# Kernel tuning notes

Measured on AMD Instinct MI355X. Metric: run time of the kernel, lower is better.

The kernel has to match this reference:

```python
import jax, jax.numpy as jnp
import numpy as np

N_NODES = 50000
N_EDGES = 1600000
D_IN = 128
D_HID = 128
D_OUT = 3
EPS = 1e-5


def setup_inputs() -> dict:
    key = jax.random.key(0)
    ks = jax.random.split(key, 16)
    def lin(k, fi, fo):
        s = 1.0 / np.sqrt(fi)
        return jax.random.uniform(k, (fi, fo), jnp.float32, -s, s)
    inp = {
        "x": jax.random.normal(ks[0], (N_NODES, D_IN), jnp.float32),
        "edge_index": jax.random.randint(ks[1], (2, N_EDGES), 0, N_NODES, jnp.int32),
        "W1": lin(ks[2], D_IN, D_HID), "b1": jnp.zeros((D_HID,), jnp.float32),
        "W2": lin(ks[3], D_HID, D_HID), "b2": jnp.zeros((D_HID,), jnp.float32),
        "W3": lin(ks[4], D_HID, D_HID), "b3": jnp.zeros((D_HID,), jnp.float32),
        "g1": jnp.ones((D_HID,), jnp.float32), "beta1": jnp.zeros((D_HID,), jnp.float32),
        "g2": jnp.ones((D_HID,), jnp.float32), "beta2": jnp.zeros((D_HID,), jnp.float32),
        "Wp1": lin(ks[5], D_HID, D_HID), "bp1": jnp.zeros((D_HID,), jnp.float32),
        "Wp2": lin(ks[6], D_HID, D_OUT), "bp2": jnp.zeros((D_OUT,), jnp.float32),
    }
    return inp


def _gcn_norm(edge_index, n):
    # add self-loops, symmetric normalization (PyG GCNConv default)
    loops = jnp.arange(n, dtype=edge_index.dtype)
    row = jnp.concatenate([edge_index[0], loops])  # source
    col = jnp.concatenate([edge_index[1], loops])  # target
    deg = jax.ops.segment_sum(jnp.ones_like(col, jnp.float32), col, num_segments=n)
    dinv = jnp.where(deg > 0, jax.lax.rsqrt(deg), 0.0)
    norm = dinv[row] * dinv[col]  # [E+N]
    return row, col, norm


def _gcn_conv(x, W, b, row, col, norm, n):
    h = x @ W                                # [N, F]
    msg = h[row] * norm[:, None]             # [E+N, F] gather
    out = jax.ops.segment_sum(msg, col, num_segments=n)  # scatter-add
    return out + b


def _layernorm(x, g, beta):
    mu = jnp.mean(x, axis=-1, keepdims=True)
    var = jnp.var(x, axis=-1, keepdims=True)
    return (x - mu) * jax.lax.rsqrt(var + EPS) * g + beta


def reference(x, edge_index, W1, b1, W2, b2, W3, b3, g1, beta1, g2, beta2, Wp1, bp1, Wp2, bp2):
    n = x.shape[0]
    row, col, norm = _gcn_norm(edge_index, n)
    # layer 0
    h = _gcn_conv(x, W1, b1, row, col, norm, n)
    h = _layernorm(jax.nn.relu(h), g1, beta1)  # dropout = identity (eval mode)
    # layer 1
    h = _gcn_conv(h, W2, b2, row, col, norm, n)
    h = _layernorm(jax.nn.relu(h), g2, beta2)
    # layer 2 (no layernorm)
    h = _gcn_conv(h, W3, b3, row, col, norm, n)
    h = jax.nn.relu(h)
    # post-MP MLP head (dropout = identity in eval)
    h = h @ Wp1 + bp1
    return h @ Wp2 + bp2
```

## Files before the change

### kernel.cpp

```cpp
#include <hip/hip_runtime.h>
#include <hip/hip_bf16.h>

#define EPS_LN 1e-5f
#define NB    256
#define SEGCAP 16384

typedef int ivec4 __attribute__((ext_vector_type(4)));


__global__ __launch_bounds__(256) void bucket_hist(const int* __restrict__ col,
                                                   int* __restrict__ chunkBH,
                                                   int E, int per, int nbuck) {
    __shared__ int hist[256];
    int t = threadIdx.x;
    hist[t] = 0;
    __syncthreads();
    int s0 = blockIdx.x * per;
    int s1 = s0 + per; if (s1 > E) s1 = E;
    if (s0 < s1) {
        int q0 = s0 >> 2, q1 = s1 >> 2;
        for (int i = q0 + t; i < q1; i += 256) {
            ivec4 c = __builtin_nontemporal_load((const ivec4*)col + i);
            atomicAdd(&hist[c.x >> 8], 1);
            atomicAdd(&hist[c.y >> 8], 1);
            atomicAdd(&hist[c.z >> 8], 1);
            atomicAdd(&hist[c.w >> 8], 1);
        }
        for (int i = (q1 << 2) + t; i < s1; i += 256)
            atomicAdd(&hist[col[i] >> 8], 1);
    }
    __syncthreads();
    if (t < nbuck) chunkBH[blockIdx.x * 256 + t] = hist[t];
}

__global__ __launch_bounds__(256) void bucket_scan(int* __restrict__ chunkBH,
                                                   int* __restrict__ bucketStart,
                                                   int* __restrict__ rowPtr,
                                                   int E, int n, int nbuck, int nb) {
    __shared__ int tot[256];
    int t = threadIdx.x;
    int run = 0;
    if (t < nbuck) {
        for (int k0 = 0; k0 < nb; k0 += 16) {
            int v[16];
#pragma unroll
            for (int j = 0; j < 16; j++)
                v[j] = (k0 + j < nb) ? chunkBH[(k0 + j) * 256 + t] : 0;
#pragma unroll
            for (int j = 0; j < 16; j++) {
                int tv = v[j];
                if (k0 + j < nb) chunkBH[(k0 + j) * 256 + t] = run;
                run += tv;
            }
        }
    }
    tot[t] = run;
    __syncthreads();
    for (int d = 1; d < 256; d <<= 1) {
        int add = (t >= d) ? tot[t - d] : 0;
        __syncthreads();
        tot[t] += add;
        __syncthreads();
    }
    if (t < nbuck) bucketStart[t] = tot[t] - run;
    if (t == 0) { bucketStart[nbuck] = E; rowPtr[n] = E; }
}

__global__ __launch_bounds__(256) void scatter_pairs(const int* __restrict__ row,
                                                     const int* __restrict__ col,
                                                     const int* __restrict__ chunkBH,
                                                     const int* __restrict__ bucketStart,
                                                     unsigned long long* __restrict__ tmp,
                                                     int E, int per, int nbuck) {
    __shared__ int curs[256];
    int t = threadIdx.x;
    int k = blockIdx.x;
    curs[t] = (t < nbuck) ? (chunkBH[k * 256 + t] + bucketStart[t]) : 0;
    __syncthreads();
    int s0 = k * per;
    int s1 = s0 + per; if (s1 > E) s1 = E;
    if (s0 >= s1) return;
    int q0 = s0 >> 2, q1 = s1 >> 2;
    for (int i = q0 + t; i < q1; i += 256) {
        ivec4 c4 = __builtin_nontemporal_load((const ivec4*)col + i);
        ivec4 r4 = __builtin_nontemporal_load((const ivec4*)row + i);
        int p0 = atomicAdd(&curs[c4.x >> 8], 1);
        tmp[p0] = ((unsigned long long)(unsigned)c4.x << 32) | (unsigned)r4.x;
        int p1 = atomicAdd(&curs[c4.y >> 8], 1);
        tmp[p1] = ((unsigned long long)(unsigned)c4.y << 32) | (unsigned)r4.y;
        int p2 = atomicAdd(&curs[c4.z >> 8], 1);
        tmp[p2] = ((unsigned long long)(unsigned)c4.z << 32) | (unsigned)r4.z;
        int p3 = atomicAdd(&curs[c4.w >> 8], 1);
        tmp[p3] = ((unsigned long long)(unsigned)c4.w << 32) | (unsigned)r4.w;
    }
    for (int i = (q1 << 2) + t; i < s1; i += 256) {
        int c = col[i], r = row[i];
        int p = atomicAdd(&curs[c >> 8], 1);
        tmp[p] = ((unsigned long long)(unsigned)c << 32) | (unsigned)r;
    }
}

__global__ __launch_bounds__(256) void bucket_fill(const unsigned long long* __restrict__ tmp,
                                                   const int* __restrict__ bucketStart,
                                                   int* __restrict__ rowPtr,
                                                   float* __restrict__ dinv,
                                                   int* __restrict__ srcList,
                                                   int n) {
    __shared__ int cnt[256];
    __shared__ int cur[256];
    __shared__ int seg[SEGCAP];
    int b = blockIdx.x, t = threadIdx.x;
    int node0 = b << 8;
    int s0 = bucketStart[b], s1 = bucketStart[b + 1];
    int len = s1 - s0;
    cnt[t] = 0;
    __syncthreads();
    for (int i = s0 + t; i < s1; i += 256) {
        int c = (int)(tmp[i] >> 32);
        atomicAdd(&cnt[c - node0], 1);
    }
    __syncthreads();
    int v = cnt[t];
    cur[t] = v;
    __syncthreads();
    for (int d = 1; d < 256; d <<= 1) {
        int add = (t >= d) ? cur[t - d] : 0;
        __syncthreads();
        cur[t] += add;
        __syncthreads();
    }
    int excl = cur[t] - v;
    int node = node0 + t;
    if (node < n) {
        rowPtr[node] = s0 + excl;
        dinv[node] = rsqrtf((float)v + 1.0f);
    }
    cur[t] = excl;
    __syncthreads();
    if (len <= SEGCAP) {
        for (int i = s0 + t; i < s1; i += 256) {
            unsigned long long p = tmp[i];
            int c = (int)(p >> 32);
            int r = (int)(p & 0xffffffffu);
            int pos = atomicAdd(&cur[c - node0], 1);
            seg[pos] = r;
        }
        __syncthreads();
        for (int i = t; i < len; i += 256)
            srcList[s0 + i] = seg[i];
    } else {
        for (int i = s0 + t; i < s1; i += 256) {
            unsigned long long p = tmp[i];
            int c = (int)(p >> 32);
            int r = (int)(p & 0xffffffffu);
            int pos = atomicAdd(&cur[c - node0], 1);
            srcList[s0 + pos] = r;
        }
    }
}

__global__ __launch_bounds__(256) void gemm_hb(const float* __restrict__ A,
                                               const float* __restrict__ W,
                                               const float* __restrict__ dinv,
                                               unsigned short* __restrict__ Cb,
                                               int n) {
    __shared__ float As[16][68];
    __shared__ float Ws[16][144];

    const int tx = threadIdx.x;
    const int row0 = blockIdx.x * 64;
    const int jg = (tx & 15) * 8;
    const int ig = (tx >> 4) * 4;
    const int js = jg + ((jg >> 5) << 2);

    const int ar  = tx >> 2;
    const int ac4 = (tx & 3) * 4;
    const int growA = row0 + ar;
    const float* Ap = A + (size_t)growA * 128 + ac4;

    float acc[4][8];
#pragma unroll
    for (int r = 0; r < 4; r++)
#pragma unroll
        for (int c = 0; c < 8; c++) acc[r][c] = 0.f;

    for (int k0 = 0; k0 < 128; k0 += 16) {
        float4 va = make_float4(0.f, 0.f, 0.f, 0.f);
        if (growA < n) va = *(const float4*)(Ap + k0);
        As[ac4 + 0][ar] = va.x;
        As[ac4 + 1][ar] = va.y;
        As[ac4 + 2][ar] = va.z;
        As[ac4 + 3][ar] = va.w;
#pragma unroll
        for (int q = 0; q < 2; q++) {
            int f = tx * 2 + q;
            int kr = f >> 5;
            int c4 = (f & 31) * 4;
            int cs = c4 + ((c4 >> 5) << 2);
            *(float4*)&Ws[kr][cs] = *(const float4*)(W + (size_t)(k0 + kr) * 128 + c4);
        }
        __syncthreads();
#pragma unroll
        for (int kk = 0; kk < 16; kk++) {
            float4 a4 = *(const float4*)&As[kk][ig];
            float4 w0 = *(const float4*)&Ws[kk][js];
            float4 w1 = *(const float4*)&Ws[kk][js + 4];
            float av[4] = {a4.x, a4.y, a4.z, a4.w};
            float wv[8] = {w0.x, w0.y, w0.z, w0.w, w1.x, w1.y, w1.z, w1.w};
#pragma unroll
            for (int r = 0; r < 4; r++)
#pragma unroll
                for (int c = 0; c < 8; c++) acc[r][c] += av[r] * wv[c];
        }
        __syncthreads();
    }

#pragma unroll
    for (int r = 0; r < 4; r++) {
        int grow = row0 + ig + r;
        if (grow < n) {
            float dr = dinv[grow];
            ushort4 u0, u1;
            __hip_bfloat16 t;
            t = __float2bfloat16(acc[r][0] * dr); u0.x = *(unsigned short*)&t;
            t = __float2bfloat16(acc[r][1] * dr); u0.y = *(unsigned short*)&t;
            t = __float2bfloat16(acc[r][2] * dr); u0.z = *(unsigned short*)&t;
            t = __float2bfloat16(acc[r][3] * dr); u0.w = *(unsigned short*)&t;
            t = __float2bfloat16(acc[r][4] * dr); u1.x = *(unsigned short*)&t;
            t = __float2bfloat16(acc[r][5] * dr); u1.y = *(unsigned short*)&t;
            t = __float2bfloat16(acc[r][6] * dr); u1.z = *(unsigned short*)&t;
            t = __float2bfloat16(acc[r][7] * dr); u1.w = *(unsigned short*)&t;
            *(ushort4*)(Cb + (size_t)grow * 128 + jg)     = u0;
            *(ushort4*)(Cb + (size_t)grow * 128 + jg + 4) = u1;
        }
    }
}

#define BF_LO(u) __uint_as_float((u) << 16)
#define BF_HI(u) __uint_as_float((u) & 0xffff0000u)

template<bool DO_LN>
__global__ __launch_bounds__(128) void agg_post(const unsigned int* __restrict__ hb,
                                                const int* __restrict__ rowPtr,
                                                const int* __restrict__ srcList,
                                                const float* __restrict__ dinv,
                                                const float* __restrict__ b,
                                                const float* __restrict__ g,
                                                const float* __restrict__ beta,
                                                float* __restrict__ out, int n) {
    int wid = (blockIdx.x * 128 + threadIdx.x) >> 6;
    int lane = threadIdx.x & 63;
    if (wid >= n) return;
    int h = lane & 15;
    int gg = lane >> 4;
    int e0 = rowPtr[wid], e1 = rowPtr[wid + 1];
    float dc = dinv[wid];
    const uint4* hb4 = (const uint4*)hb;

    uint4 us = hb4[(size_t)wid * 16 + h];

    float a[8];
#pragma unroll
    for (int j = 0; j < 8; j++) a[j] = 0.f;

    int idx0 = (e0 + gg < e1) ? srcList[e0 + gg] : -1;
    int idx1 = (e0 + 4 + gg < e1) ? srcList[e0 + 4 + gg] : -1;

    int e = e0;
    for (; e + 8 <= e1; e += 8) {
        int ni0 = (e + 8 + gg < e1) ? srcList[e + 8 + gg] : -1;
        int ni1 = (e + 12 + gg < e1) ? srcList[e + 12 + gg] : -1;
        uint4 u0 = hb4[(size_t)idx0 * 16 + h];
        uint4 u1 = hb4[(size_t)idx1 * 16 + h];
        a[0] += BF_LO(u0.x); a[1] += BF_HI(u0.x);
        a[2] += BF_LO(u0.y); a[3] += BF_HI(u0.y);
        a[4] += BF_LO(u0.z); a[5] += BF_HI(u0.z);
        a[6] += BF_LO(u0.w); a[7] += BF_HI(u0.w);
        a[0] += BF_LO(u1.x); a[1] += BF_HI(u1.x);
        a[2] += BF_LO(u1.y); a[3] += BF_HI(u1.y);
        a[4] += BF_LO(u1.z); a[5] += BF_HI(u1.z);
        a[6] += BF_LO(u1.w); a[7] += BF_HI(u1.w);
        idx0 = ni0; idx1 = ni1;
    }
    if (idx0 >= 0) {
        uint4 u = hb4[(size_t)idx0 * 16 + h];
        a[0] += BF_LO(u.x); a[1] += BF_HI(u.x);
        a[2] += BF_LO(u.y); a[3] += BF_HI(u.y);
        a[4] += BF_LO(u.z); a[5] += BF_HI(u.z);
        a[6] += BF_LO(u.w); a[7] += BF_HI(u.w);
    }
    if (idx1 >= 0) {
        uint4 u = hb4[(size_t)idx1 * 16 + h];
        a[0] += BF_LO(u.x); a[1] += BF_HI(u.x);
        a[2] += BF_LO(u.y); a[3] += BF_HI(u.y);
        a[4] += BF_LO(u.z); a[5] += BF_HI(u.z);
        a[6] += BF_LO(u.w); a[7] += BF_HI(u.w);
    }

#pragma unroll
    for (int j = 0; j < 8; j++) {
        a[j] += __shfl_xor(a[j], 16, 64);
        a[j] += __shfl_xor(a[j], 32, 64);
    }

    a[0] += BF_LO(us.x); a[1] += BF_HI(us.x);
    a[2] += BF_LO(us.y); a[3] += BF_HI(us.y);
    a[4] += BF_LO(us.z); a[5] += BF_HI(us.z);
    a[6] += BF_LO(us.w); a[7] += BF_HI(us.w);

    float4 bv0 = *(const float4*)(b + h * 8);
    float4 bv1 = *(const float4*)(b + h * 8 + 4);
    a[0] = fmaxf(a[0] * dc + bv0.x, 0.f);
    a[1] = fmaxf(a[1] * dc + bv0.y, 0.f);
    a[2] = fmaxf(a[2] * dc + bv0.z, 0.f);
    a[3] = fmaxf(a[3] * dc + bv0.w, 0.f);
    a[4] = fmaxf(a[4] * dc + bv1.x, 0.f);
    a[5] = fmaxf(a[5] * dc + bv1.y, 0.f);
    a[6] = fmaxf(a[6] * dc + bv1.z, 0.f);
    a[7] = fmaxf(a[7] * dc + bv1.w, 0.f);

    if (DO_LN) {
        float s = ((a[0] + a[1]) + (a[2] + a[3])) + ((a[4] + a[5]) + (a[6] + a[7]));
#pragma unroll
        for (int m = 8; m >= 1; m >>= 1) s += __shfl_xor(s, m, 64);
        float mu = s * (1.f / 128.f);
        float sq = 0.f;
        float d[8];
#pragma unroll
        for (int j = 0; j < 8; j++) { d[j] = a[j] - mu; sq += d[j] * d[j]; }
#pragma unroll
        for (int m = 8; m >= 1; m >>= 1) sq += __shfl_xor(sq, m, 64);
        float rs = rsqrtf(sq * (1.f / 128.f) + EPS_LN);
        float4 gv0 = *(const float4*)(g + h * 8);
        float4 gv1 = *(const float4*)(g + h * 8 + 4);
        float4 bt0 = *(const float4*)(beta + h * 8);
        float4 bt1 = *(const float4*)(beta + h * 8 + 4);
        a[0] = d[0] * rs * gv0.x + bt0.x;
        a[1] = d[1] * rs * gv0.y + bt0.y;
        a[2] = d[2] * rs * gv0.z + bt0.z;
        a[3] = d[3] * rs * gv0.w + bt0.w;
        a[4] = d[4] * rs * gv1.x + bt1.x;
        a[5] = d[5] * rs * gv1.y + bt1.y;
        a[6] = d[6] * rs * gv1.z + bt1.z;
        a[7] = d[7] * rs * gv1.w + bt1.w;
    }
    if (gg == 0) {
        *(float4*)(out + (size_t)wid * 128 + h * 8)     = make_float4(a[0], a[1], a[2], a[3]);
        *(float4*)(out + (size_t)wid * 128 + h * 8 + 4) = make_float4(a[4], a[5], a[6], a[7]);
    }
}

__global__ __launch_bounds__(128) void head_collapse(const float* __restrict__ Wp1,
                                                     const float* __restrict__ bp1,
                                                     const float* __restrict__ Wp2,
                                                     const float* __restrict__ bp2,
                                                     float* __restrict__ Weff,
                                                     float* __restrict__ beff) {
    __shared__ float w2[384];
    int t = threadIdx.x;
    w2[t] = Wp2[t]; w2[t + 128] = Wp2[t + 128]; w2[t + 256] = Wp2[t + 256];
    __syncthreads();
    float p0 = 0.f, p1 = 0.f, p2 = 0.f;
    const float* wr = Wp1 + (size_t)t * 128;
    for (int k = 0; k < 128; k++) {
        float v = wr[k];
        p0 += v * w2[k * 3 + 0];
        p1 += v * w2[k * 3 + 1];
        p2 += v * w2[k * 3 + 2];
    }
    Weff[t * 3 + 0] = p0; Weff[t * 3 + 1] = p1; Weff[t * 3 + 2] = p2;
    if (t == 0) {
        float q0 = bp2[0], q1 = bp2[1], q2 = bp2[2];
        for (int k = 0; k < 128; k++) {
            float v = bp1[k];
            q0 += v * w2[k * 3 + 0];
            q1 += v * w2[k * 3 + 1];
            q2 += v * w2[k * 3 + 2];
        }
        beff[0] = q0; beff[1] = q1; beff[2] = q2;
    }
}

__global__ __launch_bounds__(256) void nhead_f32(const float* __restrict__ hp,
                                                 const float* __restrict__ W,
                                                 const float* __restrict__ b,
                                                 float* __restrict__ out, int n) {
    __shared__ float Ws[384];
    int t = threadIdx.x;
    if (t < 192) { Ws[t] = W[t]; Ws[t + 192] = W[t + 192]; }
    __syncthreads();
    int i = blockIdx.x * 256 + t;
    if (i >= n) return;
    float p0 = b[0], p1 = b[1], p2 = b[2];
    const float4* h4 = (const float4*)(hp + (size_t)i * 128);
#pragma unroll
    for (int k4 = 0; k4 < 32; k4++) {
        float4 v = h4[k4];
        const float* w = &Ws[k4 * 12];
        p0 += v.x * w[0] + v.y * w[3] + v.z * w[6] + v.w * w[9];
        p1 += v.x * w[1] + v.y * w[4] + v.z * w[7] + v.w * w[10];
        p2 += v.x * w[2] + v.y * w[5] + v.z * w[8] + v.w * w[11];
    }
    out[(size_t)i * 3 + 0] = p0;
    out[(size_t)i * 3 + 1] = p1;
    out[(size_t)i * 3 + 2] = p2;
}

extern "C" void kernel_launch(void* const* d_in, const int* in_sizes, int n_in,
                              void* d_out, int out_size, void* d_ws, size_t ws_size,
                              hipStream_t stream) {
    const float* x   = (const float*)d_in[0];
    const int* ei    = (const int*)d_in[1];
    const float* W1  = (const float*)d_in[2];
    const float* b1  = (const float*)d_in[3];
    const float* W2  = (const float*)d_in[4];
    const float* b2  = (const float*)d_in[5];
    const float* W3  = (const float*)d_in[6];
    const float* b3  = (const float*)d_in[7];
    const float* g1  = (const float*)d_in[8];
    const float* be1 = (const float*)d_in[9];
    const float* g2  = (const float*)d_in[10];
    const float* be2 = (const float*)d_in[11];
    const float* Wp1 = (const float*)d_in[12];
    const float* bp1 = (const float*)d_in[13];
    const float* Wp2 = (const float*)d_in[14];
    const float* bp2 = (const float*)d_in[15];
    float* out = (float*)d_out;

    const int n = in_sizes[0] / 128;
    const int E = in_sizes[1] / 2;
    const int* row = ei;
    const int* col = ei + E;

    char* ws = (char*)d_ws;
    size_t nA  = ((size_t)n * 4 + 255) & ~(size_t)255;
    size_t nA1 = ((size_t)(n + 1) * 4 + 255) & ~(size_t)255;
    size_t eA  = ((size_t)E * 4 + 255) & ~(size_t)255;
    size_t hbA = ((size_t)n * 128 * 2 + 255) & ~(size_t)255;
    int*   rowPtr  = (int*)ws;
    float* dinvp   = (float*)(ws + nA1);
    int*   srcList = (int*)(ws + nA1 + nA);
    unsigned short* hb = (unsigned short*)(ws + nA1 + nA + eA);
    float* bufA    = (float*)(ws + nA1 + nA + eA + hbA);
    float* bufB    = bufA + (size_t)n * 128;
    float* Weff    = bufB + (size_t)n * 128;
    float* beff    = Weff + 384;
    unsigned long long* tmp = (unsigned long long*)bufA;
    int* chunkBH    = (int*)((char*)bufA + 2 * eA);
    int* bucketStart = (int*)((char*)bufA + 2 * eA + (size_t)NB * 256 * 4);

    const int nbuck = (n + 255) >> 8;
    const int per   = (((E + NB - 1) / NB) + 15) & ~15;
    const int gemmBlocks = (n + 63) / 64;
    const int nodeWaveBlocks = (n + 1) / 2;
    const int nodeBlocks = (n + 255) / 256;

    bucket_hist<<<NB, 256, 0, stream>>>(col, chunkBH, E, per, nbuck);
    bucket_scan<<<1, 256, 0, stream>>>(chunkBH, bucketStart, rowPtr, E, n, nbuck, NB);
    scatter_pairs<<<NB, 256, 0, stream>>>(row, col, chunkBH, bucketStart, tmp, E, per, nbuck);
    bucket_fill<<<nbuck, 256, 0, stream>>>(tmp, bucketStart, rowPtr, dinvp, srcList, n);
    head_collapse<<<1, 128, 0, stream>>>(Wp1, bp1, Wp2, bp2, Weff, beff);

    gemm_hb<<<gemmBlocks, 256, 0, stream>>>(x, W1, dinvp, hb, n);
    agg_post<true><<<nodeWaveBlocks, 128, 0, stream>>>((const unsigned int*)hb,
                                                       rowPtr, srcList, dinvp,
                                                       b1, g1, be1, bufB, n);
    gemm_hb<<<gemmBlocks, 256, 0, stream>>>(bufB, W2, dinvp, hb, n);
    agg_post<true><<<nodeWaveBlocks, 128, 0, stream>>>((const unsigned int*)hb,
                                                       rowPtr, srcList, dinvp,
                                                       b2, g2, be2, bufA, n);
    gemm_hb<<<gemmBlocks, 256, 0, stream>>>(bufA, W3, dinvp, hb, n);
    agg_post<false><<<nodeWaveBlocks, 128, 0, stream>>>((const unsigned int*)hb,
                                                        rowPtr, srcList, dinvp,
                                                        b3, b3, b3, bufB, n);
    nhead_f32<<<nodeBlocks, 256, 0, stream>>>(bufB, Weff, beff, out, n);
}
```

Before: 415.7 us.

## Fuse aggregation+LayerNorm with next-layer GEMM, and fold head into final aggregation

Each aggregation kernel for layers 0 and 1 now also computes the next layer's 128x128 GEMM in the same block. It stages 64 normalized rows in shared memory and writes bf16 pre-scaled features directly, so the fp32 intermediate round trip through global memory and two separate gemm launches go away. The last aggregation also applies the collapsed MLP head per node, which removes the fp32 bufB write and the nhead kernel. In exchange, blocks grow to 512 threads with about 44KB of shared memory, each wave processes 8 nodes sequentially, and the GEMM runs behind a barrier, so occupancy and latency hiding for the gather may suffer.

After: 466.9 us. 1.12x slower.

```diff
diff --git a/kernel.cpp b/kernel.cpp
--- a/kernel.cpp
+++ b/kernel.cpp
@@ -239,24 +239,198 @@
 #define BF_LO(u) __uint_as_float((u) << 16)
 #define BF_HI(u) __uint_as_float((u) & 0xffff0000u)
 
-template<bool DO_LN>
-__global__ __launch_bounds__(128) void agg_post(const unsigned int* __restrict__ hb,
-                                                const int* __restrict__ rowPtr,
-                                                const int* __restrict__ srcList,
-                                                const float* __restrict__ dinv,
-                                                const float* __restrict__ b,
-                                                const float* __restrict__ g,
-                                                const float* __restrict__ beta,
-                                                float* __restrict__ out, int n) {
-    int wid = (blockIdx.x * 128 + threadIdx.x) >> 6;
-    int lane = threadIdx.x & 63;
+__global__ __launch_bounds__(512) void fused_agg_gemm(
+        const unsigned int* __restrict__ hb,
+        const int* __restrict__ rowPtr,
+        const int* __restrict__ srcList,
+        const float* __restrict__ dinv,
+        const float* __restrict__ b,
+        const float* __restrict__ g,
+        const float* __restrict__ beta,
+        const float* __restrict__ W,
+        unsigned short* __restrict__ hbOut,
+        int n) {
+    __shared__ float Asf[128][68];
+    __shared__ float Ws[16][144];
+
+    const int tx = threadIdx.x;
+    const int base = blockIdx.x * 64;
+    const int wv = tx >> 6;
+    const int lane = tx & 63;
+    const int h = lane & 15;
+    const int gg = lane >> 4;
+    const uint4* hb4 = (const uint4*)hb;
+
+    for (int it = 0; it < 8; ++it) {
+        int wid = base + wv * 8 + it;
+        if (wid >= n) break;
+        int e0 = rowPtr[wid], e1 = rowPtr[wid + 1];
+        float dc = dinv[wid];
+        uint4 us = hb4[(size_t)wid * 16 + h];
+
+        float a[8];
+#pragma unroll
+        for (int j = 0; j < 8; j++) a[j] = 0.f;
+
+        int idx0 = (e0 + gg < e1) ? srcList[e0 + gg] : -1;
+        int idx1 = (e0 + 4 + gg < e1) ? srcList[e0 + 4 + gg] : -1;
+        int e = e0;
+        for (; e + 8 <= e1; e += 8) {
+            int ni0 = (e + 8 + gg < e1) ? srcList[e + 8 + gg] : -1;
+            int ni1 = (e + 12 + gg < e1) ? srcList[e + 12 + gg] : -1;
+            uint4 u0 = hb4[(size_t)idx0 * 16 + h];
+            uint4 u1 = hb4[(size_t)idx1 * 16 + h];
+            a[0] += BF_LO(u0.x); a[1] += BF_HI(u0.x);
+            a[2] += BF_LO(u0.y); a[3] += BF_HI(u0.y);
+            a[4] += BF_LO(u0.z); a[5] += BF_HI(u0.z);
+            a[6] += BF_LO(u0.w); a[7] += BF_HI(u0.w);
+            a[0] += BF_LO(u1.x); a[1] += BF_HI(u1.x);
+            a[2] += BF_LO(u1.y); a[3] += BF_HI(u1.y);
+            a[4] += BF_LO(u1.z); a[5] += BF_HI(u1.z);
+            a[6] += BF_LO(u1.w); a[7] += BF_HI(u1.w);
+            idx0 = ni0; idx1 = ni1;
+        }
+        if (idx0 >= 0) {
+            uint4 u = hb4[(size_t)idx0 * 16 + h];
+            a[0] += BF_LO(u.x); a[1] += BF_HI(u.x);
+            a[2] += BF_LO(u.y); a[3] += BF_HI(u.y);
+            a[4] += BF_LO(u.z); a[5] += BF_HI(u.z);
+            a[6] += BF_LO(u.w); a[7] += BF_HI(u.w);
+        }
+        if (idx1 >= 0) {
+            uint4 u = hb4[(size_t)idx1 * 16 + h];
+            a[0] += BF_LO(u.x); a[1] += BF_HI(u.x);
+            a[2] += BF_LO(u.y); a[3] += BF_HI(u.y);
+            a[4] += BF_LO(u.z); a[5] += BF_HI(u.z);
+            a[6] += BF_LO(u.w); a[7] += BF_HI(u.w);
+        }
+#pragma unroll
+        for (int j = 0; j < 8; j++) {
+            a[j] += __shfl_xor(a[j], 16, 64);
+            a[j] += __shfl_xor(a[j], 32, 64);
+        }
+        a[0] += BF_LO(us.x); a[1] += BF_HI(us.x);
+        a[2] += BF_LO(us.y); a[3] += BF_HI(us.y);
+        a[4] += BF_LO(us.z); a[5] += BF_HI(us.z);
+        a[6] += BF_LO(us.w); a[7] += BF_HI(us.w);
+
+        float4 bv0 = *(const float4*)(b + h * 8);
+        float4 bv1 = *(const float4*)(b + h * 8 + 4);
+        a[0] = fmaxf(a[0] * dc + bv0.x, 0.f);
+        a[1] = fmaxf(a[1] * dc + bv0.y, 0.f);
+        a[2] = fmaxf(a[2] * dc + bv0.z, 0.f);
+        a[3] = fmaxf(a[3] * dc + bv0.w, 0.f);
+        a[4] = fmaxf(a[4] * dc + bv1.x, 0.f);
+        a[5] = fmaxf(a[5] * dc + bv1.y, 0.f);
+        a[6] = fmaxf(a[6] * dc + bv1.z, 0.f);
+        a[7] = fmaxf(a[7] * dc + bv1.w, 0.f);
+
+        float s = ((a[0] + a[1]) + (a[2] + a[3])) + ((a[4] + a[5]) + (a[6] + a[7]));
+#pragma unroll
+        for (int m = 8; m >= 1; m >>= 1) s += __shfl_xor(s, m, 64);
+        float mu = s * (1.f / 128.f);
+        float sq = 0.f;
+        float d[8];
+#pragma unroll
+        for (int j = 0; j < 8; j++) { d[j] = a[j] - mu; sq += d[j] * d[j]; }
+#pragma unroll
+        for (int m = 8; m >= 1; m >>= 1) sq += __shfl_xor(sq, m, 64);
+        float rs = rsqrtf(sq * (1.f / 128.f) + EPS_LN);
+        float4 gv0 = *(const float4*)(g + h * 8);
+        float4 gv1 = *(const float4*)(g + h * 8 + 4);
+        float4 bt0 = *(const float4*)(beta + h * 8);
+        float4 bt1 = *(const float4*)(beta + h * 8 + 4);
+        a[0] = d[0] * rs * gv0.x + bt0.x;
+        a[1] = d[1] * rs * gv0.y + bt0.y;
+        a[2] = d[2] * rs * gv0.z + bt0.z;
+        a[3] = d[3] * rs * gv0.w + bt0.w;
+        a[4] = d[4] * rs * gv1.x + bt1.x;
+        a[5] = d[5] * rs * gv1.y + bt1.y;
+        a[6] = d[6] * rs * gv1.z + bt1.z;
+        a[7] = d[7] * rs * gv1.w + bt1.w;
+
+        int c = wv * 8 + it;
+        int f0 = 8 * h + 2 * gg;
+        Asf[f0][c]     = a[2 * gg];
+        Asf[f0 + 1][c] = a[2 * gg + 1];
+    }
+    __syncthreads();
+
+    const int jg = (tx & 15) * 8;
+    const int ig = (tx >> 4) * 2;
+    const int js = jg + ((jg >> 5) << 2);
+    float acc[2][8];
+#pragma unroll
+    for (int r = 0; r < 2; r++)
+#pragma unroll
+        for (int cc = 0; cc < 8; cc++) acc[r][cc] = 0.f;
+
+    for (int k0 = 0; k0 < 128; k0 += 16) {
+        {
+            int kr = tx >> 5;
+            int c4 = (tx & 31) * 4;
+            int cs = c4 + ((c4 >> 5) << 2);
+            *(float4*)&Ws[kr][cs] = *(const float4*)(W + (size_t)(k0 + kr) * 128 + c4);
+        }
+        __syncthreads();
+#pragma unroll
+        for (int kk = 0; kk < 16; kk++) {
+            float2 a2 = *(const float2*)&Asf[k0 + kk][ig];
+            float4 w0 = *(const float4*)&Ws[kk][js];
+            float4 w1 = *(const float4*)&Ws[kk][js + 4];
+            float wvv[8] = {w0.x, w0.y, w0.z, w0.w, w1.x, w1.y, w1.z, w1.w};
+#pragma unroll
+            for (int cc = 0; cc < 8; cc++) {
+                acc[0][cc] += a2.x * wvv[cc];
+                acc[1][cc] += a2.y * wvv[cc];
+            }
+        }
+        __syncthreads();
+    }
+
+#pragma unroll
+    for (int r = 0; r < 2; r++) {
+        int grow = base + ig + r;
+        if (grow < n) {
+            float dr = dinv[grow];
+            ushort4 u0, u1;
+            __hip_bfloat16 t;
+            t = __float2bfloat16(acc[r][0] * dr); u0.x = *(unsigned short*)&t;
+            t = __float2bfloat16(acc[r][1] * dr); u0.y = *(unsigned short*)&t;
+            t = __float2bfloat16(acc[r][2] * dr); u0.z = *(unsigned short*)&t;
+            t = __float2bfloat16(acc[r][3] * dr); u0.w = *(unsigned short*)&t;
+            t = __float2bfloat16(acc[r][4] * dr); u1.x = *(unsigned short*)&t;
+            t = __float2bfloat16(acc[r][5] * dr); u1.y = *(unsigned short*)&t;
+            t = __float2bfloat16(acc[r][6] * dr); u1.z = *(unsigned short*)&t;
+            t = __float2bfloat16(acc[r][7] * dr); u1.w = *(unsigned short*)&t;
+            *(ushort4*)(hbOut + (size_t)grow * 128 + jg)     = u0;
+            *(ushort4*)(hbOut + (size_t)grow * 128 + jg + 4) = u1;
+        }
+    }
+}
+
+__global__ __launch_bounds__(128) void agg_head(
+        const unsigned int* __restrict__ hb,
+        const int* __restrict__ rowPtr,
+        const int* __restrict__ srcList,
+        const float* __restrict__ dinv,
+        const float* __restrict__ b,
+        const float* __restrict__ Weff,
+        const float* __restrict__ beff,
+        float* __restrict__ out, int n) {
+    __shared__ float Wl[384];
+    int tt = threadIdx.x;
+    Wl[tt] = Weff[tt]; Wl[tt + 128] = Weff[tt + 128]; Wl[tt + 256] = Weff[tt + 256];
+    __syncthreads();
+
+    int wid = (blockIdx.x * 128 + tt) >> 6;
+    int lane = tt & 63;
     if (wid >= n) return;
     int h = lane & 15;
     int gg = lane >> 4;
     int e0 = rowPtr[wid], e1 = rowPtr[wid + 1];
     float dc = dinv[wid];
     const uint4* hb4 = (const uint4*)hb;
-
     uint4 us = hb4[(size_t)wid * 16 + h];
 
     float a[8];
@@ -265,7 +439,6 @@
 
     int idx0 = (e0 + gg < e1) ? srcList[e0 + gg] : -1;
     int idx1 = (e0 + 4 + gg < e1) ? srcList[e0 + 4 + gg] : -1;
-
     int e = e0;
     for (; e + 8 <= e1; e += 8) {
         int ni0 = (e + 8 + gg < e1) ? srcList[e + 8 + gg] : -1;
@@ -296,13 +469,11 @@
         a[4] += BF_LO(u.z); a[5] += BF_HI(u.z);
         a[6] += BF_LO(u.w); a[7] += BF_HI(u.w);
     }
-
 #pragma unroll
     for (int j = 0; j < 8; j++) {
         a[j] += __shfl_xor(a[j], 16, 64);
         a[j] += __shfl_xor(a[j], 32, 64);
     }
-
     a[0] += BF_LO(us.x); a[1] += BF_HI(us.x);
     a[2] += BF_LO(us.y); a[3] += BF_HI(us.y);
     a[4] += BF_LO(us.z); a[5] += BF_HI(us.z);
@@ -319,34 +490,24 @@
     a[6] = fmaxf(a[6] * dc + bv1.z, 0.f);
     a[7] = fmaxf(a[7] * dc + bv1.w, 0.f);
 
-    if (DO_LN) {
-        float s = ((a[0] + a[1]) + (a[2] + a[3])) + ((a[4] + a[5]) + (a[6] + a[7]));
-#pragma unroll
-        for (int m = 8; m >= 1; m >>= 1) s += __shfl_xor(s, m, 64);
-        float mu = s * (1.f / 128.f);
-        float sq = 0.f;
-        float d[8];
-#pragma unroll
-        for (int j = 0; j < 8; j++) { d[j] = a[j] - mu; sq += d[j] * d[j]; }
-#pragma unroll
-        for (int m = 8; m >= 1; m >>= 1) sq += __shfl_xor(sq, m, 64);
-        float rs = rsqrtf(sq * (1.f / 128.f) + EPS_LN);
-        float4 gv0 = *(const float4*)(g + h * 8);
-        float4 gv1 = *(const float4*)(g + h * 8 + 4);
-        float4 bt0 = *(const float4*)(beta + h * 8);
-        float4 bt1 = *(const float4*)(beta + h * 8 + 4);
-        a[0] = d[0] * rs * gv0.x + bt0.x;
-        a[1] = d[1] * rs * gv0.y + bt0.y;
-        a[2] = d[2] * rs * gv0.z + bt0.z;
-        a[3] = d[3] * rs * gv0.w + bt0.w;
-        a[4] = d[4] * rs * gv1.x + bt1.x;
-        a[5] = d[5] * rs * gv1.y + bt1.y;
-        a[6] = d[6] * rs * gv1.z + bt1.z;
-        a[7] = d[7] * rs * gv1.w + bt1.w;
-    }
-    if (gg == 0) {
-        *(float4*)(out + (size_t)wid * 128 + h * 8)     = make_float4(a[0], a[1], a[2], a[3]);
-        *(float4*)(out + (size_t)wid * 128 + h * 8 + 4) = make_float4(a[4], a[5], a[6], a[7]);
+    float p0 = 0.f, p1 = 0.f, p2 = 0.f;
+#pragma unroll
+    for (int j = 0; j < 8; j++) {
+        const float* w = &Wl[(8 * h + j) * 3];
+        p0 += a[j] * w[0];
+        p1 += a[j] * w[1];
+        p2 += a[j] * w[2];
+    }
+#pragma unroll
+    for (int m = 8; m >= 1; m >>= 1) {
+        p0 += __shfl_xor(p0, m, 64);
+        p1 += __shfl_xor(p1, m, 64);
+        p2 += __shfl_xor(p2, m, 64);
+    }
+    if (lane == 0) {
+        out[(size_t)wid * 3 + 0] = p0 + beff[0];
+        out[(size_t)wid * 3 + 1] = p1 + beff[1];
+        out[(size_t)wid * 3 + 2] = p2 + beff[2];
     }
 }
 
@@ -379,31 +540,6 @@
         }
         beff[0] = q0; beff[1] = q1; beff[2] = q2;
     }
-}
-
-__global__ __launch_bounds__(256) void nhead_f32(const float* __restrict__ hp,
-                                                 const float* __restrict__ W,
-                                                 const float* __restrict__ b,
-                                                 float* __restrict__ out, int n) {
-    __shared__ float Ws[384];
-    int t = threadIdx.x;
-    if (t < 192) { Ws[t] = W[t]; Ws[t + 192] = W[t + 192]; }
-    __syncthreads();
-    int i = blockIdx.x * 256 + t;
-    if (i >= n) return;
-    float p0 = b[0], p1 = b[1], p2 = b[2];
-    const float4* h4 = (const float4*)(hp + (size_t)i * 128);
-#pragma unroll
-    for (int k4 = 0; k4 < 32; k4++) {
-        float4 v = h4[k4];
-        const float* w = &Ws[k4 * 12];
-        p0 += v.x * w[0] + v.y * w[3] + v.z * w[6] + v.w * w[9];
-        p1 += v.x * w[1] + v.y * w[4] + v.z * w[7] + v.w * w[10];
-        p2 += v.x * w[2] + v.y * w[5] + v.z * w[8] + v.w * w[11];
-    }
-    out[(size_t)i * 3 + 0] = p0;
-    out[(size_t)i * 3 + 1] = p1;
-    out[(size_t)i * 3 + 2] = p2;
 }
 
 extern "C" void kernel_launch(void* const* d_in, const int* in_sizes, int n_in,
@@ -436,24 +572,24 @@
     size_t nA  = ((size_t)n * 4 + 255) & ~(size_t)255;
     size_t nA1 = ((size_t)(n + 1) * 4 + 255) & ~(size_t)255;
     size_t eA  = ((size_t)E * 4 + 255) & ~(size_t)255;
-    size_t hbA = ((size_t)n * 128 * 2 + 255) & ~(size_t)255;
+    size_t hbA_sz = ((size_t)n * 128 * 2 + 255) & ~(size_t)255;
     int*   rowPtr  = (int*)ws;
     float* dinvp   = (float*)(ws + nA1);
     int*   srcList = (int*)(ws + nA1 + nA);
-    unsigned short* hb = (unsigned short*)(ws + nA1 + nA + eA);
-    float* bufA    = (float*)(ws + nA1 + nA + eA + hbA);
+    unsigned short* hbA = (unsigned short*)(ws + nA1 + nA + eA);
+    float* bufA    = (float*)(ws + nA1 + nA + eA + hbA_sz);
     float* bufB    = bufA + (size_t)n * 128;
-    float* Weff    = bufB + (size_t)n * 128;
-    float* beff    = Weff + 384;
+    unsigned short* hbB = (unsigned short*)bufA;
+    float* Weff    = bufB;
+    float* beff    = bufB + 384;
     unsigned long long* tmp = (unsigned long long*)bufA;
     int* chunkBH    = (int*)((char*)bufA + 2 * eA);
     int* bucketStart = (int*)((char*)bufA + 2 * eA + (size_t)NB * 256 * 4);
 
     const int nbuck = (n + 255) >> 8;
     const int per   = (((E + NB - 1) / NB) + 15) & ~15;
-    const int gemmBlocks = (n + 63) / 64;
+    const int tileBlocks = (n + 63) / 64;
     const int nodeWaveBlocks = (n + 1) / 2;
-    const int nodeBlocks = (n + 255) / 256;
 
     bucket_hist<<<NB, 256, 0, stream>>>(col, chunkBH, E, per, nbuck);
     bucket_scan<<<1, 256, 0, stream>>>(chunkBH, bucketStart, rowPtr, E, n, nbuck, NB);
@@ -461,17 +597,14 @@
     bucket_fill<<<nbuck, 256, 0, stream>>>(tmp, bucketStart, rowPtr, dinvp, srcList, n);
     head_collapse<<<1, 128, 0, stream>>>(Wp1, bp1, Wp2, bp2, Weff, beff);
 
-    gemm_hb<<<gemmBlocks, 256, 0, stream>>>(x, W1, dinvp, hb, n);
-    agg_post<true><<<nodeWaveBlocks, 128, 0, stream>>>((const unsigned int*)hb,
-                                                       rowPtr, srcList, dinvp,
-                                                       b1, g1, be1, bufB, n);
-    gemm_hb<<<gemmBlocks, 256, 0, stream>>>(bufB, W2, dinvp, hb, n);
-    agg_post<true><<<nodeWaveBlocks, 128, 0, stream>>>((const unsigned int*)hb,
-                                                       rowPtr, srcList, dinvp,
-                                                       b2, g2, be2, bufA, n);
-    gemm_hb<<<gemmBlocks, 256, 0, stream>>>(bufA, W3, dinvp, hb, n);
-    agg_post<false><<<nodeWaveBlocks, 128, 0, stream>>>((const unsigned int*)hb,
-                                                        rowPtr, srcList, dinvp,
-                                                        b3, b3, b3, bufB, n);
-    nhead_f32<<<nodeBlocks, 256, 0, stream>>>(bufB, Weff, beff, out, n);
-}
+    gemm_hb<<<tileBlocks, 256, 0, stream>>>(x, W1, dinvp, hbA, n);
+    fused_agg_gemm<<<tileBlocks, 512, 0, stream>>>((const unsigned int*)hbA,
+                                                   rowPtr, srcList, dinvp,
+                                                   b1, g1, be1, W2, hbB, n);
+    fused_agg_gemm<<<tileBlocks, 512, 0, stream>>>((const unsigned int*)hbB,
+                                                   rowPtr, srcList, dinvp,
+                                                   b2, g2, be2, W3, hbA, n);
+    agg_head<<<nodeWaveBlocks, 128, 0, stream>>>((const unsigned int*)hbA,
+                                                 rowPtr, srcList, dinvp,
+                                                 b3, Weff, beff, out, n);
+}
```
